# Optimization experiments

Measured on AMD Instinct MI355X. Metric: run time of the kernel, lower is better.

The kernel has to match this reference:

```python
import jax, jax.numpy as jnp
import numpy as np

B, T, DIM, HEADS, DH = 4, 2048, 1024, 16, 64
MAX_SEQ_LEN = 2048


def setup_inputs() -> dict:
    key = jax.random.key(0)
    k1, k2, k3, k4 = jax.random.split(key, 4)
    x = jax.random.normal(k1, (B, T, DIM), dtype=jnp.float32)
    W_qkv = jax.random.normal(k2, (DIM, 3 * HEADS * DH), dtype=jnp.float32) * (DIM ** -0.5)
    W_0 = jax.random.normal(k3, (HEADS * DH, DIM), dtype=jnp.float32) * ((HEADS * DH) ** -0.5)
    rel_bias = jax.random.normal(k4, (2 * MAX_SEQ_LEN - 1, HEADS), dtype=jnp.float32) * 0.02
    return {"x": x, "W_qkv": W_qkv, "W_0": W_0, "rel_bias": rel_bias}


def reference(x, W_qkv, W_0, rel_bias):
    b, t, dim = x.shape
    heads = rel_bias.shape[1]
    dh = W_qkv.shape[1] // (3 * heads)
    scale = dh ** -0.5

    qkv = x @ W_qkv  # (b, t, 3*heads*dh), feature layout is (d, k, h): d slowest, h fastest
    qkv = qkv.reshape(b, t, dh, 3, heads)
    qkv = jnp.transpose(qkv, (3, 0, 4, 1, 2))  # (3, b, h, t, d)
    q, k, v = qkv[0], qkv[1], qkv[2]

    scores = jnp.einsum('bhid,bhjd->bhij', q, k) * scale  # (b, h, t, t)

    causal = jnp.tril(jnp.ones((t, t), dtype=bool))
    scores = jnp.where(causal[None, None], scores, -jnp.inf)

    # relative position bias: index = j - i + t - 1
    rel_idx = jnp.arange(t)[None, :] - jnp.arange(t)[:, None] + (t - 1)  # (t, t)
    bias = rel_bias[rel_idx]  # (t, t, heads)
    scores = scores + jnp.transpose(bias, (2, 0, 1))[None]

    attn = jax.nn.softmax(scores, axis=-1)
    out = jnp.einsum('bhij,bhjd->bhid', attn, v)  # (b, h, t, d)
    out = jnp.transpose(out, (0, 2, 1, 3)).reshape(b, t, heads * dh)
    return out @ W_0
```

## Files before the change

kernel.cpp:

```cpp
#include <hip/hip_runtime.h>
#include <hip/hip_bf16.h>
#include <stdint.h>

#define B_ 4
#define T_ 2048
#define NH 16
#define DH 64
#define DIM 1024
#define NF 3072
#define QKS 2048

typedef unsigned short u16;
typedef uint32_t u32;
typedef __bf16 bf16;
typedef bf16 bf16x8 __attribute__((ext_vector_type(8)));
typedef float f32x4 __attribute__((ext_vector_type(4)));
typedef u16 u16x8 __attribute__((ext_vector_type(8)));
typedef u16 u16x4 __attribute__((ext_vector_type(4)));

__device__ __forceinline__ u16 f2bf(float f) {
    u32 u = __builtin_bit_cast(u32, f);
    u = (u + 0x7fffu + ((u >> 16) & 1u)) >> 16;
    return (u16)u;
}

__device__ __forceinline__ float exp2f_fast(float x) {
#if __has_builtin(__builtin_amdgcn_exp2f)
    return __builtin_amdgcn_exp2f(x);
#else
    return exp2f(x);
#endif
}

#define GLOAD16(g, l)                                                          \
    __builtin_amdgcn_global_load_lds(                                          \
        (const __attribute__((address_space(1))) u32*)(g),                     \
        (__attribute__((address_space(3))) u32*)(l), 16, 0, 0)

__global__ __launch_bounds__(256) void prep_k(const float* __restrict__ x,
                                              const float* __restrict__ Wqkv,
                                              const float* __restrict__ W0,
                                              const float* __restrict__ rb,
                                              u16* __restrict__ xb,
                                              u16* __restrict__ WqkvT,
                                              u16* __restrict__ W0T,
                                              u16* __restrict__ rbT2,
                                              u16* __restrict__ rbT2s) {
    __shared__ float tile[32][33];
    const int bid = blockIdx.x;
    if (bid < 4096) {
        const bool perm = bid < 3072;
        const float* src = perm ? Wqkv : W0;
        u16* dst = perm ? WqkvT : W0T;
        const int N = perm ? NF : DIM;
        const int r2 = perm ? bid : bid - 3072;
        const int nb = perm ? 96 : 32;
        const int n0 = (r2 % nb) * 32, k0 = (r2 / nb) * 32;
        int c = threadIdx.x & 31, r0 = threadIdx.x >> 5;
#pragma unroll
        for (int i = 0; i < 4; i++) {
            int r = r0 + i * 8;
            tile[r][c] = src[(size_t)(k0 + r) * N + n0 + c];
        }
        __syncthreads();
#pragma unroll
        for (int i = 0; i < 4; i++) {
            int r = r0 + i * 8;
            int n = n0 + r;
            int nd;
            if (perm) {
                int d = n / 48, rem = n - d * 48;
                int kk = rem >> 4, h = rem & 15;
                nd = kk * 1024 + h * 64 + d;
            } else {
                nd = n;
            }
            dst[(size_t)nd * DIM + k0 + c] = f2bf(tile[c][r]);
        }
    } else if (bid < 4352) {
        int i = (bid - 4096) * 256 + threadIdx.x;
        int h = i >> 12, d = i & 4095;
        float v = (d <= 2047) ? rb[(size_t)d * NH + h] * 1.44269504f : -1e30f;
        rbT2[i] = __builtin_bit_cast(u16, (bf16)v);
        int d2 = d + 1;
        float v2 = (d2 <= 2047) ? rb[(size_t)d2 * NH + h] * 1.44269504f : -1e30f;
        rbT2s[i] = __builtin_bit_cast(u16, (bf16)v2);
    } else {
        int i = (bid - 4352) * 256 + threadIdx.x;
        const float4* s = (const float4*)x + (size_t)i * 2;
        float4 a = s[0], b = s[1];
        u16x8 o;
        o[0]=f2bf(a.x); o[1]=f2bf(a.y); o[2]=f2bf(a.z); o[3]=f2bf(a.w);
        o[4]=f2bf(b.x); o[5]=f2bf(b.y); o[6]=f2bf(b.z); o[7]=f2bf(b.w);
        *(u16x8*)(xb + (size_t)i * 8) = o;
    }
}


template <int OUTMODE>
__global__ __launch_bounds__(256, 2) void gemm_bt_k(const u16* __restrict__ A,
                                                    const u16* __restrict__ Bt,
                                                    void* __restrict__ Cout,
                                                    u16* __restrict__ Vt,
                                                    int M, int N, int K) {
    __shared__ __align__(16) u16 As[128 * 64];
    __shared__ __align__(16) u16 Bs[128 * 64];
    const int tid = threadIdx.x;
    const int wave = tid >> 6, lane = tid & 63;
    const int bm = blockIdx.x, bn = blockIdx.y;
    const int wr = (wave >> 1) * 64, wc = (wave & 1) * 64;
    const int lrow = lane & 15, g4 = lane >> 4;
    const int srow8 = lane >> 3;
    const int scs = (lane & 7) ^ srow8;
    const u16* Ab = A + (size_t)(bm * 128 + wave * 32) * K;
    const u16* Bb = Bt + (size_t)(bn * 128 + wave * 32) * K;
    u16* AsW = As + wave * 2048;
    u16* BsW = Bs + wave * 2048;
    const bool vt = (OUTMODE == 1) && (bn >= 16);
    f32x4 acc[4][4] = {};

    for (int k0 = 0; k0 < K; k0 += 64) {
        __syncthreads();
#pragma unroll
        for (int g = 0; g < 4; g++) {
            GLOAD16(Ab + (size_t)(g * 8 + srow8) * K + k0 + scs * 8, AsW + g * 512);
            GLOAD16(Bb + (size_t)(g * 8 + srow8) * K + k0 + scs * 8, BsW + g * 512);
        }
        __syncthreads();
#pragma unroll
        for (int kk2 = 0; kk2 < 2; kk2++) {
            bf16x8 af[4], bfr[4];
#pragma unroll
            for (int i = 0; i < 4; i++)
                af[i] = *(const bf16x8*)&As[(wr + i * 16 + lrow) * 64 +
                                            (((kk2 * 4 + g4) ^ (lrow & 7)) * 8)];
#pragma unroll
            for (int j = 0; j < 4; j++)
                bfr[j] = *(const bf16x8*)&Bs[(wc + j * 16 + lrow) * 64 +
                                             (((kk2 * 4 + g4) ^ (lrow & 7)) * 8)];
            if (vt) {
#pragma unroll
                for (int i = 0; i < 4; i++)
#pragma unroll
                    for (int j = 0; j < 4; j++)
                        acc[i][j] = __builtin_amdgcn_mfma_f32_16x16x32_bf16(
                            bfr[j], af[i], acc[i][j], 0, 0, 0);
            } else {
#pragma unroll
                for (int i = 0; i < 4; i++)
#pragma unroll
                    for (int j = 0; j < 4; j++)
                        acc[i][j] = __builtin_amdgcn_mfma_f32_16x16x32_bf16(
                            af[i], bfr[j], acc[i][j], 0, 0, 0);
            }
        }
    }

    const int crow = (lane >> 4) * 4, ccol = lane & 15;
    if (vt) {
#pragma unroll
        for (int i = 0; i < 4; i++)
#pragma unroll
            for (int j = 0; j < 4; j++) {
                int gm = bm * 128 + wr + i * 16 + ccol;
                int b = gm >> 11, tt = gm & 2047;
#pragma unroll
                for (int r = 0; r < 4; r++) {
                    int f = (bn - 16) * 128 + wc + j * 16 + crow + r;
                    int h = f >> 6, d = f & 63;
                    Vt[(((size_t)(b * NH + h)) * DH + d) * T_ + tt] =
                        f2bf(acc[i][j][r]);
                }
            }
    } else {
#pragma unroll
        for (int i = 0; i < 4; i++)
#pragma unroll
            for (int j = 0; j < 4; j++) {
                int gm = bm * 128 + wr + i * 16 + crow;
                int gn = bn * 128 + wc + j * 16 + ccol;
#pragma unroll
                for (int r = 0; r < 4; r++) {
                    if (OUTMODE == 1)
                        ((u16*)Cout)[(size_t)(gm + r) * N + gn] = f2bf(acc[i][j][r]);
                    else
                        ((float*)Cout)[(size_t)(gm + r) * N + gn] = acc[i][j][r];
                }
            }
    }
}

__global__ __launch_bounds__(256, 2) void flash_attn_k(const u16* __restrict__ qkF,
                                                       const u16* __restrict__ Vt,
                                                       const u16* __restrict__ rbT2,
                                                       const u16* __restrict__ rbT2s,
                                                       u16* __restrict__ O) {
    __shared__ __align__(16) u16 Ks[2][64 * 64];
    __shared__ __align__(16) u16 Vs[2][64 * 64];
    __shared__ __align__(16) u16 Ps[4][2][16 * 64];
    __shared__ __align__(16) u16 rbs2a[4096];
    __shared__ __align__(16) u16 rbs2b[4096];
    const int tid = threadIdx.x, wave = tid >> 6, lane = tid & 63;
    const int Lid = blockIdx.x;
    const int c = Lid & 7, u = Lid >> 3;
    const int bh = ((u & 7) << 3) | c;
    const int pair = u >> 3;
    const int h = bh & 15, b = bh >> 4;
    const int l15 = lane & 15, g4 = lane >> 4;
    const float SC2 = 0.125f * 1.44269504f;

    {
        *(u16x8*)&rbs2a[tid * 8] = *(const u16x8*)&rbT2[(size_t)h * 4096 + tid * 8];
        *(u16x8*)&rbs2a[2048 + tid * 8] = *(const u16x8*)&rbT2[(size_t)h * 4096 + 2048 + tid * 8];
        *(u16x8*)&rbs2b[tid * 8] = *(const u16x8*)&rbT2s[(size_t)h * 4096 + tid * 8];
        *(u16x8*)&rbs2b[2048 + tid * 8] = *(const u16x8*)&rbT2s[(size_t)h * 4096 + 2048 + tid * 8];
    }

    const size_t trow = (size_t)b * T_;
    u16* pwA = &Ps[wave][0][0];
    u16* pwB = &Ps[wave][1][0];
    const int lrow8 = lane >> 3, lch = lane & 7;
    const int swz = lch ^ lrow8;
    const u16* kg0 = &qkF[(trow + wave * 16 + lrow8) * QKS + 1024 + h * 64 + swz * 8];
    const u16* kg1 = kg0 + (size_t)8 * QKS;
    const u16* vg0 = &Vt[((size_t)bh * DH + wave * 16 + lrow8) * T_ + swz * 8];
    const u16* vg1 = vg0 + (size_t)8 * T_;

#define STAGE_KV(j0n, buf)                                                     \
    do {                                                                       \
        GLOAD16(kg0 + (size_t)(j0n) * QKS, &Ks[buf][(wave * 16) * 64]);        \
        GLOAD16(kg1 + (size_t)(j0n) * QKS, &Ks[buf][(wave * 16 + 8) * 64]);    \
        GLOAD16(vg0 + (j0n), &Vs[buf][(wave * 16) * 64]);                      \
        GLOAD16(vg1 + (j0n), &Vs[buf][(wave * 16 + 8) * 64]);                  \
    } while (0)

    STAGE_KV(0, 0);
    __syncthreads();
    int cur = 0;

    for (int half = 0; half < 2; half++) {
        const int blk = half ? 15 - pair : pair;
        const int qbA = blk * 128 + wave * 16;
        const int qbB = qbA + 64;
        bf16x8 aqA[2], aqB[2];
        aqA[0] = *(const bf16x8*)&qkF[(trow + qbA + l15) * QKS + h * 64 + g4 * 8];
        aqA[1] = *(const bf16x8*)&qkF[(trow + qbA + l15) * QKS + h * 64 + 32 + g4 * 8];
        aqB[0] = *(const bf16x8*)&qkF[(trow + qbB + l15) * QKS + h * 64 + g4 * 8];
        aqB[1] = *(const bf16x8*)&qkF[(trow + qbB + l15) * QKS + h * 64 + 32 + g4 * 8];

        const int ibA = 2047 - l15 + g4 * 4 - qbA;
        const u32* b32A = (const u32*)((ibA & 1) ? &rbs2b[ibA - 1] : &rbs2a[ibA]);
        const u32* b32B = b32A - 32;

        f32x4 oaccA[4] = {}, oaccB[4] = {};
        float lA = 0.f, lB = 0.f;

        const int jtmax = 2 * blk + 1;
        for (int jt = 0; jt <= jtmax; jt++) {
            const int j0 = jt * 64;
            const int j0n = (jt + 1 <= jtmax) ? (jt + 1) * 64 : (half == 0 ? 0 : -1);
            if (j0n >= 0) STAGE_KV(j0n, cur ^ 1);
            const u16* KsC = &Ks[cur][0];
            const u16* VsC = &Vs[cur][0];
            f32x4 sA[4], sB[4];
#pragma unroll
            for (int ni = 0; ni < 4; ni++) {
                f32x4 z = {};
                sA[ni] = z;
                sB[ni] = z;
            }
            __builtin_amdgcn_s_setprio(1);
#pragma unroll
            for (int ni = 0; ni < 4; ni++) {
                int arow = ni * 16 + l15;
#pragma unroll
                for (int kk = 0; kk < 2; kk++) {
                    int ch = kk * 4 + g4;
                    bf16x8 ak = *(const bf16x8*)&KsC[arow * 64 + ((ch ^ (arow & 7)) * 8)];
                    sA[ni] = __builtin_amdgcn_mfma_f32_16x16x32_bf16(ak, aqA[kk], sA[ni], 0, 0, 0);
                    sB[ni] = __builtin_amdgcn_mfma_f32_16x16x32_bf16(ak, aqB[kk], sB[ni], 0, 0, 0);
                }
            }
            __builtin_amdgcn_s_setprio(0);
            const int jo = j0 >> 1;
            {
                float su = 0.f;
#pragma unroll
                for (int ni = 0; ni < 4; ni++) {
                    u32 w0 = b32A[jo + ni * 8];
                    u32 w1 = b32A[jo + ni * 8 + 1];
                    float e0 = exp2f_fast(fmaf(sA[ni][0], SC2, __builtin_bit_cast(float, w0 << 16)));
                    float e1 = exp2f_fast(fmaf(sA[ni][1], SC2, __builtin_bit_cast(float, w0 & 0xffff0000u)));
                    float e2 = exp2f_fast(fmaf(sA[ni][2], SC2, __builtin_bit_cast(float, w1 << 16)));
                    float e3 = exp2f_fast(fmaf(sA[ni][3], SC2, __builtin_bit_cast(float, w1 & 0xffff0000u)));
                    su += (e0 + e1) + (e2 + e3);
                    u16x4 pk;
                    pk[0] = __builtin_bit_cast(u16, (bf16)e0);
                    pk[1] = __builtin_bit_cast(u16, (bf16)e1);
                    pk[2] = __builtin_bit_cast(u16, (bf16)e2);
                    pk[3] = __builtin_bit_cast(u16, (bf16)e3);
                    int colb = ni * 16 + g4 * 4;
                    int ch = colb >> 3, co = colb & 7;
                    *(u16x4*)&pwA[l15 * 64 + ((ch ^ (l15 & 7)) * 8) + co] = pk;
                }
                su += __shfl_xor(su, 16);
                su += __shfl_xor(su, 32);
                lA += su;
            }
            {
                float su = 0.f;
#pragma unroll
                for (int ni = 0; ni < 4; ni++) {
                    u32 w0 = b32B[jo + ni * 8];
                    u32 w1 = b32B[jo + ni * 8 + 1];
                    float e0 = exp2f_fast(fmaf(sB[ni][0], SC2, __builtin_bit_cast(float, w0 << 16)));
                    float e1 = exp2f_fast(fmaf(sB[ni][1], SC2, __builtin_bit_cast(float, w0 & 0xffff0000u)));
                    float e2 = exp2f_fast(fmaf(sB[ni][2], SC2, __builtin_bit_cast(float, w1 << 16)));
                    float e3 = exp2f_fast(fmaf(sB[ni][3], SC2, __builtin_bit_cast(float, w1 & 0xffff0000u)));
                    su += (e0 + e1) + (e2 + e3);
                    u16x4 pk;
                    pk[0] = __builtin_bit_cast(u16, (bf16)e0);
                    pk[1] = __builtin_bit_cast(u16, (bf16)e1);
                    pk[2] = __builtin_bit_cast(u16, (bf16)e2);
                    pk[3] = __builtin_bit_cast(u16, (bf16)e3);
                    int colb = ni * 16 + g4 * 4;
                    int ch = colb >> 3, co = colb & 7;
                    *(u16x4*)&pwB[l15 * 64 + ((ch ^ (l15 & 7)) * 8) + co] = pk;
                }
                su += __shfl_xor(su, 16);
                su += __shfl_xor(su, 32);
                lB += su;
            }
            bf16x8 bpA[2], bpB[2];
#pragma unroll
            for (int kk = 0; kk < 2; kk++) {
                int ch = kk * 4 + g4;
                int off = l15 * 64 + ((ch ^ (l15 & 7)) * 8);
                bpA[kk] = *(const bf16x8*)&pwA[off];
                bpB[kk] = *(const bf16x8*)&pwB[off];
            }
            __builtin_amdgcn_s_setprio(1);
#pragma unroll
            for (int di = 0; di < 4; di++) {
                int vrow = di * 16 + l15;
#pragma unroll
                for (int kk = 0; kk < 2; kk++) {
                    int ch = kk * 4 + g4;
                    bf16x8 av = *(const bf16x8*)&VsC[vrow * 64 + ((ch ^ (vrow & 7)) * 8)];
                    oaccA[di] = __builtin_amdgcn_mfma_f32_16x16x32_bf16(av, bpA[kk], oaccA[di], 0, 0, 0);
                    oaccB[di] = __builtin_amdgcn_mfma_f32_16x16x32_bf16(av, bpB[kk], oaccB[di], 0, 0, 0);
                }
            }
            __builtin_amdgcn_s_setprio(0);
            __syncthreads();
            cur ^= 1;
        }
        {
            float inv = 1.0f / lA;
            u16* orow = &O[((size_t)b * T_ + qbA + l15) * (NH * DH) + h * DH];
#pragma unroll
            for (int di = 0; di < 4; di++) {
                u16x4 ov;
#pragma unroll
                for (int r = 0; r < 4; r++)
                    ov[r] = __builtin_bit_cast(u16, (bf16)(oaccA[di][r] * inv));
                *(u16x4*)&orow[di * 16 + g4 * 4] = ov;
            }
        }
        {
            float inv = 1.0f / lB;
            u16* orow = &O[((size_t)b * T_ + qbB + l15) * (NH * DH) + h * DH];
#pragma unroll
            for (int di = 0; di < 4; di++) {
                u16x4 ov;
#pragma unroll
                for (int r = 0; r < 4; r++)
                    ov[r] = __builtin_bit_cast(u16, (bf16)(oaccB[di][r] * inv));
                *(u16x4*)&orow[di * 16 + g4 * 4] = ov;
            }
        }
    }
#undef STAGE_KV
}


extern "C" void kernel_launch(void* const* d_in, const int* in_sizes, int n_in,
                              void* d_out, int out_size, void* d_ws, size_t ws_size,
                              hipStream_t stream) {
    const float* x    = (const float*)d_in[0];
    const float* Wqkv = (const float*)d_in[1];
    const float* W0   = (const float*)d_in[2];
    const float* rb   = (const float*)d_in[3];
    char* ws = (char*)d_ws;

    u16*   xb    = (u16*)(ws + 0);
    u16*   WqkvT = (u16*)(ws + 16777216);
    u16*   W0T   = (u16*)(ws + 23068672);
    u16*   rbT2  = (u16*)(ws + 25165824);
    u16*   rbT2s = (u16*)(ws + 25296896);
    u16*   qkF   = (u16*)(ws + 25427968);
    u16*   attnO = (u16*)(ws + 58982400);
    u16*   Vtb   = (u16*)(ws + 75759616);

    prep_k<<<8448, 256, 0, stream>>>(x, Wqkv, W0, rb, xb, WqkvT, W0T, rbT2, rbT2s);

    gemm_bt_k<1><<<dim3((B_ * T_) / 128, NF / 128), 256, 0, stream>>>(
        xb, WqkvT, qkF, Vtb, B_ * T_, QKS, DIM);

    flash_attn_k<<<512, 256, 0, stream>>>(qkF, Vtb, rbT2, rbT2s, attnO);

    gemm_bt_k<0><<<dim3((B_ * T_) / 128, DIM / 128), 256, 0, stream>>>(
        attnO, W0T, d_out, nullptr, B_ * T_, DIM, DIM);
}
```

Baseline: 162.4 us.

## Split paired causal query blocks into separate workgroups and drop KV double buffering

The attention kernel no longer has each workgroup handle two query blocks (pair and 15-pair) to balance causal work. It launches 1024 workgroups, one 128-row query block each, scheduled from largest to smallest block. K/V staging drops from double buffers to a single buffer, with syncs before and after each load, which removes the overlap of the next tile's load with compute. The aim is more parallelism and less LDS per block, at the cost of exposed global-to-LDS latency and extra barriers.

```diff
diff --git a/kernel.cpp b/kernel.cpp
--- a/kernel.cpp
+++ b/kernel.cpp
@@ -195,8 +195,8 @@
                                                        const u16* __restrict__ rbT2,
                                                        const u16* __restrict__ rbT2s,
                                                        u16* __restrict__ O) {
-    __shared__ __align__(16) u16 Ks[2][64 * 64];
-    __shared__ __align__(16) u16 Vs[2][64 * 64];
+    __shared__ __align__(16) u16 Ks[64 * 64];
+    __shared__ __align__(16) u16 Vs[64 * 64];
     __shared__ __align__(16) u16 Ps[4][2][16 * 64];
     __shared__ __align__(16) u16 rbs2a[4096];
     __shared__ __align__(16) u16 rbs2b[4096];
@@ -204,7 +204,7 @@
     const int Lid = blockIdx.x;
     const int c = Lid & 7, u = Lid >> 3;
     const int bh = ((u & 7) << 3) | c;
-    const int pair = u >> 3;
+    const int blk = 15 - (u >> 3);
     const int h = bh & 15, b = bh >> 4;
     const int l15 = lane & 15, g4 = lane >> 4;
     const float SC2 = 0.125f * 1.44269504f;
@@ -226,158 +226,148 @@
     const u16* vg0 = &Vt[((size_t)bh * DH + wave * 16 + lrow8) * T_ + swz * 8];
     const u16* vg1 = vg0 + (size_t)8 * T_;
 
-#define STAGE_KV(j0n, buf)                                                     \
+#define STAGE_KV(j0n)                                                          \
     do {                                                                       \
-        GLOAD16(kg0 + (size_t)(j0n) * QKS, &Ks[buf][(wave * 16) * 64]);        \
-        GLOAD16(kg1 + (size_t)(j0n) * QKS, &Ks[buf][(wave * 16 + 8) * 64]);    \
-        GLOAD16(vg0 + (j0n), &Vs[buf][(wave * 16) * 64]);                      \
-        GLOAD16(vg1 + (j0n), &Vs[buf][(wave * 16 + 8) * 64]);                  \
+        GLOAD16(kg0 + (size_t)(j0n) * QKS, &Ks[(wave * 16) * 64]);             \
+        GLOAD16(kg1 + (size_t)(j0n) * QKS, &Ks[(wave * 16 + 8) * 64]);         \
+        GLOAD16(vg0 + (j0n), &Vs[(wave * 16) * 64]);                           \
+        GLOAD16(vg1 + (j0n), &Vs[(wave * 16 + 8) * 64]);                       \
     } while (0)
 
-    STAGE_KV(0, 0);
-    __syncthreads();
-    int cur = 0;
-
-    for (int half = 0; half < 2; half++) {
-        const int blk = half ? 15 - pair : pair;
-        const int qbA = blk * 128 + wave * 16;
-        const int qbB = qbA + 64;
-        bf16x8 aqA[2], aqB[2];
-        aqA[0] = *(const bf16x8*)&qkF[(trow + qbA + l15) * QKS + h * 64 + g4 * 8];
-        aqA[1] = *(const bf16x8*)&qkF[(trow + qbA + l15) * QKS + h * 64 + 32 + g4 * 8];
-        aqB[0] = *(const bf16x8*)&qkF[(trow + qbB + l15) * QKS + h * 64 + g4 * 8];
-        aqB[1] = *(const bf16x8*)&qkF[(trow + qbB + l15) * QKS + h * 64 + 32 + g4 * 8];
-
-        const int ibA = 2047 - l15 + g4 * 4 - qbA;
-        const u32* b32A = (const u32*)((ibA & 1) ? &rbs2b[ibA - 1] : &rbs2a[ibA]);
-        const u32* b32B = b32A - 32;
-
-        f32x4 oaccA[4] = {}, oaccB[4] = {};
-        float lA = 0.f, lB = 0.f;
-
-        const int jtmax = 2 * blk + 1;
-        for (int jt = 0; jt <= jtmax; jt++) {
-            const int j0 = jt * 64;
-            const int j0n = (jt + 1 <= jtmax) ? (jt + 1) * 64 : (half == 0 ? 0 : -1);
-            if (j0n >= 0) STAGE_KV(j0n, cur ^ 1);
-            const u16* KsC = &Ks[cur][0];
-            const u16* VsC = &Vs[cur][0];
-            f32x4 sA[4], sB[4];
-#pragma unroll
-            for (int ni = 0; ni < 4; ni++) {
-                f32x4 z = {};
-                sA[ni] = z;
-                sB[ni] = z;
-            }
-            __builtin_amdgcn_s_setprio(1);
-#pragma unroll
-            for (int ni = 0; ni < 4; ni++) {
-                int arow = ni * 16 + l15;
-#pragma unroll
-                for (int kk = 0; kk < 2; kk++) {
-                    int ch = kk * 4 + g4;
-                    bf16x8 ak = *(const bf16x8*)&KsC[arow * 64 + ((ch ^ (arow & 7)) * 8)];
-                    sA[ni] = __builtin_amdgcn_mfma_f32_16x16x32_bf16(ak, aqA[kk], sA[ni], 0, 0, 0);
-                    sB[ni] = __builtin_amdgcn_mfma_f32_16x16x32_bf16(ak, aqB[kk], sB[ni], 0, 0, 0);
-                }
-            }
-            __builtin_amdgcn_s_setprio(0);
-            const int jo = j0 >> 1;
-            {
-                float su = 0.f;
-#pragma unroll
-                for (int ni = 0; ni < 4; ni++) {
-                    u32 w0 = b32A[jo + ni * 8];
-                    u32 w1 = b32A[jo + ni * 8 + 1];
-                    float e0 = exp2f_fast(fmaf(sA[ni][0], SC2, __builtin_bit_cast(float, w0 << 16)));
-                    float e1 = exp2f_fast(fmaf(sA[ni][1], SC2, __builtin_bit_cast(float, w0 & 0xffff0000u)));
-                    float e2 = exp2f_fast(fmaf(sA[ni][2], SC2, __builtin_bit_cast(float, w1 << 16)));
-                    float e3 = exp2f_fast(fmaf(sA[ni][3], SC2, __builtin_bit_cast(float, w1 & 0xffff0000u)));
-                    su += (e0 + e1) + (e2 + e3);
-                    u16x4 pk;
-                    pk[0] = __builtin_bit_cast(u16, (bf16)e0);
-                    pk[1] = __builtin_bit_cast(u16, (bf16)e1);
-                    pk[2] = __builtin_bit_cast(u16, (bf16)e2);
-                    pk[3] = __builtin_bit_cast(u16, (bf16)e3);
-                    int colb = ni * 16 + g4 * 4;
-                    int ch = colb >> 3, co = colb & 7;
-                    *(u16x4*)&pwA[l15 * 64 + ((ch ^ (l15 & 7)) * 8) + co] = pk;
-                }
-                su += __shfl_xor(su, 16);
-                su += __shfl_xor(su, 32);
-                lA += su;
-            }
-            {
-                float su = 0.f;
-#pragma unroll
-                for (int ni = 0; ni < 4; ni++) {
-                    u32 w0 = b32B[jo + ni * 8];
-                    u32 w1 = b32B[jo + ni * 8 + 1];
-                    float e0 = exp2f_fast(fmaf(sB[ni][0], SC2, __builtin_bit_cast(float, w0 << 16)));
-                    float e1 = exp2f_fast(fmaf(sB[ni][1], SC2, __builtin_bit_cast(float, w0 & 0xffff0000u)));
-                    float e2 = exp2f_fast(fmaf(sB[ni][2], SC2, __builtin_bit_cast(float, w1 << 16)));
-                    float e3 = exp2f_fast(fmaf(sB[ni][3], SC2, __builtin_bit_cast(float, w1 & 0xffff0000u)));
-                    su += (e0 + e1) + (e2 + e3);
-                    u16x4 pk;
-                    pk[0] = __builtin_bit_cast(u16, (bf16)e0);
-                    pk[1] = __builtin_bit_cast(u16, (bf16)e1);
-                    pk[2] = __builtin_bit_cast(u16, (bf16)e2);
-                    pk[3] = __builtin_bit_cast(u16, (bf16)e3);
-                    int colb = ni * 16 + g4 * 4;
-                    int ch = colb >> 3, co = colb & 7;
-                    *(u16x4*)&pwB[l15 * 64 + ((ch ^ (l15 & 7)) * 8) + co] = pk;
-                }
-                su += __shfl_xor(su, 16);
-                su += __shfl_xor(su, 32);
-                lB += su;
-            }
-            bf16x8 bpA[2], bpB[2];
+    const int qbA = blk * 128 + wave * 16;
+    const int qbB = qbA + 64;
+    bf16x8 aqA[2], aqB[2];
+    aqA[0] = *(const bf16x8*)&qkF[(trow + qbA + l15) * QKS + h * 64 + g4 * 8];
+    aqA[1] = *(const bf16x8*)&qkF[(trow + qbA + l15) * QKS + h * 64 + 32 + g4 * 8];
+    aqB[0] = *(const bf16x8*)&qkF[(trow + qbB + l15) * QKS + h * 64 + g4 * 8];
+    aqB[1] = *(const bf16x8*)&qkF[(trow + qbB + l15) * QKS + h * 64 + 32 + g4 * 8];
+
+    const int ibA = 2047 - l15 + g4 * 4 - qbA;
+    const u32* b32A = (const u32*)((ibA & 1) ? &rbs2b[ibA - 1] : &rbs2a[ibA]);
+    const u32* b32B = b32A - 32;
+
+    f32x4 oaccA[4] = {}, oaccB[4] = {};
+    float lA = 0.f, lB = 0.f;
+
+    const int jtmax = 2 * blk + 1;
+    for (int jt = 0; jt <= jtmax; jt++) {
+        const int j0 = jt * 64;
+        __syncthreads();
+        STAGE_KV(j0);
+        __syncthreads();
+        f32x4 sA[4], sB[4];
+#pragma unroll
+        for (int ni = 0; ni < 4; ni++) {
+            f32x4 z = {};
+            sA[ni] = z;
+            sB[ni] = z;
+        }
+        __builtin_amdgcn_s_setprio(1);
+#pragma unroll
+        for (int ni = 0; ni < 4; ni++) {
+            int arow = ni * 16 + l15;
 #pragma unroll
             for (int kk = 0; kk < 2; kk++) {
                 int ch = kk * 4 + g4;
-                int off = l15 * 64 + ((ch ^ (l15 & 7)) * 8);
-                bpA[kk] = *(const bf16x8*)&pwA[off];
-                bpB[kk] = *(const bf16x8*)&pwB[off];
-            }
-            __builtin_amdgcn_s_setprio(1);
-#pragma unroll
-            for (int di = 0; di < 4; di++) {
-                int vrow = di * 16 + l15;
-#pragma unroll
-                for (int kk = 0; kk < 2; kk++) {
-                    int ch = kk * 4 + g4;
-                    bf16x8 av = *(const bf16x8*)&VsC[vrow * 64 + ((ch ^ (vrow & 7)) * 8)];
-                    oaccA[di] = __builtin_amdgcn_mfma_f32_16x16x32_bf16(av, bpA[kk], oaccA[di], 0, 0, 0);
-                    oaccB[di] = __builtin_amdgcn_mfma_f32_16x16x32_bf16(av, bpB[kk], oaccB[di], 0, 0, 0);
-                }
-            }
-            __builtin_amdgcn_s_setprio(0);
-            __syncthreads();
-            cur ^= 1;
-        }
+                bf16x8 ak = *(const bf16x8*)&Ks[arow * 64 + ((ch ^ (arow & 7)) * 8)];
+                sA[ni] = __builtin_amdgcn_mfma_f32_16x16x32_bf16(ak, aqA[kk], sA[ni], 0, 0, 0);
+                sB[ni] = __builtin_amdgcn_mfma_f32_16x16x32_bf16(ak, aqB[kk], sB[ni], 0, 0, 0);
+            }
+        }
+        __builtin_amdgcn_s_setprio(0);
+        const int jo = j0 >> 1;
         {
-            float inv = 1.0f / lA;
-            u16* orow = &O[((size_t)b * T_ + qbA + l15) * (NH * DH) + h * DH];
-#pragma unroll
-            for (int di = 0; di < 4; di++) {
-                u16x4 ov;
-#pragma unroll
-                for (int r = 0; r < 4; r++)
-                    ov[r] = __builtin_bit_cast(u16, (bf16)(oaccA[di][r] * inv));
-                *(u16x4*)&orow[di * 16 + g4 * 4] = ov;
-            }
+            float su = 0.f;
+#pragma unroll
+            for (int ni = 0; ni < 4; ni++) {
+                u32 w0 = b32A[jo + ni * 8];
+                u32 w1 = b32A[jo + ni * 8 + 1];
+                float e0 = exp2f_fast(fmaf(sA[ni][0], SC2, __builtin_bit_cast(float, w0 << 16)));
+                float e1 = exp2f_fast(fmaf(sA[ni][1], SC2, __builtin_bit_cast(float, w0 & 0xffff0000u)));
+                float e2 = exp2f_fast(fmaf(sA[ni][2], SC2, __builtin_bit_cast(float, w1 << 16)));
+                float e3 = exp2f_fast(fmaf(sA[ni][3], SC2, __builtin_bit_cast(float, w1 & 0xffff0000u)));
+                su += (e0 + e1) + (e2 + e3);
+                u16x4 pk;
+                pk[0] = __builtin_bit_cast(u16, (bf16)e0);
+                pk[1] = __builtin_bit_cast(u16, (bf16)e1);
+                pk[2] = __builtin_bit_cast(u16, (bf16)e2);
+                pk[3] = __builtin_bit_cast(u16, (bf16)e3);
+                int colb = ni * 16 + g4 * 4;
+                int ch = colb >> 3, co = colb & 7;
+                *(u16x4*)&pwA[l15 * 64 + ((ch ^ (l15 & 7)) * 8) + co] = pk;
+            }
+            su += __shfl_xor(su, 16);
+            su += __shfl_xor(su, 32);
+            lA += su;
         }
         {
-            float inv = 1.0f / lB;
-            u16* orow = &O[((size_t)b * T_ + qbB + l15) * (NH * DH) + h * DH];
-#pragma unroll
-            for (int di = 0; di < 4; di++) {
-                u16x4 ov;
-#pragma unroll
-                for (int r = 0; r < 4; r++)
-                    ov[r] = __builtin_bit_cast(u16, (bf16)(oaccB[di][r] * inv));
-                *(u16x4*)&orow[di * 16 + g4 * 4] = ov;
-            }
+            float su = 0.f;
+#pragma unroll
+            for (int ni = 0; ni < 4; ni++) {
+                u32 w0 = b32B[jo + ni * 8];
+                u32 w1 = b32B[jo + ni * 8 + 1];
+                float e0 = exp2f_fast(fmaf(sB[ni][0], SC2, __builtin_bit_cast(float, w0 << 16)));
+                float e1 = exp2f_fast(fmaf(sB[ni][1], SC2, __builtin_bit_cast(float, w0 & 0xffff0000u)));
+                float e2 = exp2f_fast(fmaf(sB[ni][2], SC2, __builtin_bit_cast(float, w1 << 16)));
+                float e3 = exp2f_fast(fmaf(sB[ni][3], SC2, __builtin_bit_cast(float, w1 & 0xffff0000u)));
+                su += (e0 + e1) + (e2 + e3);
+                u16x4 pk;
+                pk[0] = __builtin_bit_cast(u16, (bf16)e0);
+                pk[1] = __builtin_bit_cast(u16, (bf16)e1);
+                pk[2] = __builtin_bit_cast(u16, (bf16)e2);
+                pk[3] = __builtin_bit_cast(u16, (bf16)e3);
+                int colb = ni * 16 + g4 * 4;
+                int ch = colb >> 3, co = colb & 7;
+                *(u16x4*)&pwB[l15 * 64 + ((ch ^ (l15 & 7)) * 8) + co] = pk;
+            }
+            su += __shfl_xor(su, 16);
+            su += __shfl_xor(su, 32);
+            lB += su;
+        }
+        bf16x8 bpA[2], bpB[2];
+#pragma unroll
+        for (int kk = 0; kk < 2; kk++) {
+            int ch = kk * 4 + g4;
+            int off = l15 * 64 + ((ch ^ (l15 & 7)) * 8);
+            bpA[kk] = *(const bf16x8*)&pwA[off];
+            bpB[kk] = *(const bf16x8*)&pwB[off];
+        }
+        __builtin_amdgcn_s_setprio(1);
+#pragma unroll
+        for (int di = 0; di < 4; di++) {
+            int vrow = di * 16 + l15;
+#pragma unroll
+            for (int kk = 0; kk < 2; kk++) {
+                int ch = kk * 4 + g4;
+                bf16x8 av = *(const bf16x8*)&Vs[vrow * 64 + ((ch ^ (vrow & 7)) * 8)];
+                oaccA[di] = __builtin_amdgcn_mfma_f32_16x16x32_bf16(av, bpA[kk], oaccA[di], 0, 0, 0);
+                oaccB[di] = __builtin_amdgcn_mfma_f32_16x16x32_bf16(av, bpB[kk], oaccB[di], 0, 0, 0);
+            }
+        }
+        __builtin_amdgcn_s_setprio(0);
+    }
+    {
+        float inv = 1.0f / lA;
+        u16* orow = &O[((size_t)b * T_ + qbA + l15) * (NH * DH) + h * DH];
+#pragma unroll
+        for (int di = 0; di < 4; di++) {
+            u16x4 ov;
+#pragma unroll
+            for (int r = 0; r < 4; r++)
+                ov[r] = __builtin_bit_cast(u16, (bf16)(oaccA[di][r] * inv));
+            *(u16x4*)&orow[di * 16 + g4 * 4] = ov;
+        }
+    }
+    {
+        float inv = 1.0f / lB;
+        u16* orow = &O[((size_t)b * T_ + qbB + l15) * (NH * DH) + h * DH];
+#pragma unroll
+        for (int di = 0; di < 4; di++) {
+            u16x4 ov;
+#pragma unroll
+            for (int r = 0; r < 4; r++)
+                ov[r] = __builtin_bit_cast(u16, (bf16)(oaccB[di][r] * inv));
+            *(u16x4*)&orow[di * 16 + g4 * 4] = ov;
         }
     }
 #undef STAGE_KV
@@ -407,7 +397,7 @@
     gemm_bt_k<1><<<dim3((B_ * T_) / 128, NF / 128), 256, 0, stream>>>(
         xb, WqkvT, qkF, Vtb, B_ * T_, QKS, DIM);
 
-    flash_attn_k<<<512, 256, 0, stream>>>(qkF, Vtb, rbT2, rbT2s, attnO);
+    flash_attn_k<<<1024, 256, 0, stream>>>(qkF, Vtb, rbT2, rbT2s, attnO);
 
     gemm_bt_k<0><<<dim3((B_ * T_) / 128, DIM / 128), 256, 0, stream>>>(
         attnO, W0T, d_out, nullptr, B_ * T_, DIM, DIM);
```

Result: faster. 156.7 us (-3.5%).
